# Kernel optimization log

Hardware: AMD Instinct MI355X
Metric: run time of the kernel (lower is better)

## Reference

```python
import jax, jax.numpy as jnp
import numpy as np

RADIUS = 0.2
K = 32  # num_neighbors


def ball_query(centers, points, radius, k):
    """centers [B,3,M], points [B,3,N] -> int32 indices [B,M,k].
    Matches PointNet++ CUDA semantics: first k points (in original order)
    with squared distance < radius^2; slots beyond the count are filled
    with the first valid index (0 if no point is in the ball)."""
    cn = jnp.sum(centers * centers, axis=1)              # [B,M]
    pn = jnp.sum(points * points, axis=1)                # [B,N]
    cross = jnp.einsum('bdm,bdn->bmn', centers, points)  # [B,M,N]
    d2 = cn[:, :, None] + pn[:, None, :] - 2.0 * cross   # [B,M,N]
    valid = d2 < radius * radius
    # stable argsort puts valid indices first, preserving original order
    order = jnp.argsort(jnp.logical_not(valid), axis=-1, stable=True)
    idx = order[..., :k]                                  # [B,M,k]
    count = jnp.sum(valid, axis=-1, keepdims=True)        # [B,M,1]
    fill = idx[..., :1]                                   # first valid (or 0)
    return jnp.where(jnp.arange(k)[None, None, :] < count, idx, fill)


def group(features, idx):
    """features [B,C,N], idx [B,M,K] -> [B,C,M,K]."""
    return jax.vmap(lambda f, i: jnp.take(f, i, axis=1))(features, idx)


def setup_inputs() -> dict:
    key = jax.random.key(0)
    k1, k2, k3, k4 = jax.random.split(key, 4)
    B, N, M, C, CT = 8, 8192, 2048, 64, 64
    return {
        'points_coords': jax.random.uniform(k1, (B, 3, N), dtype=jnp.float32),
        'centers_coords': jax.random.uniform(k2, (B, 3, M), dtype=jnp.float32),
        'temb': jax.random.normal(k3, (B, CT, N), dtype=jnp.float32),
        'points_features': jax.random.normal(k4, (B, C, N), dtype=jnp.float32),
    }


def reference(points_coords, centers_coords, temb, points_features):
    idx = ball_query(centers_coords, points_coords, RADIUS, K)           # [B,M,K]
    neighbor_coords = group(points_coords, idx) - centers_coords[:, :, :, None]  # [B,3,M,K]
    neighbor_features = jnp.concatenate(
        [neighbor_coords, group(points_features, idx)], axis=1)          # [B,3+C,M,K]
    temb_grouped = group(temb, idx)                                      # [B,CT,M,K]
    return neighbor_features, temb_grouped
```

## Files before the change

### kernel.cpp

```cpp
#include <hip/hip_runtime.h>

#define B  8
#define N  8192
#define M  2048
#define C  64
#define CT 64
#define K  32
#define R2 0.04f

__global__ __launch_bounds__(256) void transpose_kernel(
    const float* __restrict__ points,
    const float* __restrict__ temb,
    const float* __restrict__ feats,
    float* __restrict__ pointsT,
    float* __restrict__ tembT,
    float* __restrict__ featsT)
{
    const int gx = blockIdx.x;
    if (gx < 2048) {
        const int a  = gx >> 10;
        const int tt = gx & 1023;
        const int b  = tt >> 7;
        const int n0 = (tt & 127) << 6;
        const float* src = (a ? temb : feats) + (size_t)b * 64 * N;
        float* dst = (a ? tembT : featsT) + (size_t)b * N * 64;
        __shared__ float lds[64][65];
        const int nl = threadIdx.x & 63;
        const int c0 = threadIdx.x >> 6;
        #pragma unroll
        for (int i = 0; i < 16; ++i) {
            const int c = c0 + i * 4;
            lds[c][nl] = src[(size_t)c * N + n0 + nl];
        }
        __syncthreads();
        #pragma unroll
        for (int i = 0; i < 16; ++i) {
            const int n = c0 + i * 4;
            dst[(size_t)(n0 + n) * 64 + nl] = lds[nl][n];
        }
    } else {
        const int tt = gx - 2048;
        const int b  = tt >> 5;
        const int n  = ((tt & 31) << 8) + threadIdx.x;
        const float* pc = points + (size_t)b * 3 * N;
        float* dst = pointsT + ((size_t)b * N + n) * 4;
        const float px = pc[n];
        const float py = pc[N + n];
        const float pz = pc[2 * N + n];
        dst[0] = px;
        dst[1] = py;
        dst[2] = pz;
        dst[3] = __fadd_rn(__fadd_rn(__fmul_rn(px, px), __fmul_rn(py, py)),
                           __fmul_rn(pz, pz));
    }
}

#define PROC(vv, nn)                                                          \
    do {                                                                      \
        const float cross = __fadd_rn(                                        \
            __fadd_rn(__fmul_rn(cx, (vv).x), __fmul_rn(cy, (vv).y)),          \
            __fmul_rn(cz, (vv).z));                                           \
        const float d2 = __fsub_rn(__fadd_rn(cn, (vv).w),                     \
                                   __fmul_rn(2.0f, cross));                   \
        const bool valid = d2 < R2;                                           \
        const unsigned long long mask = __ballot(valid);                      \
        if (valid) {                                                          \
            const int slot = cnt + __builtin_amdgcn_mbcnt_hi(                 \
                (unsigned)(mask >> 32),                                       \
                __builtin_amdgcn_mbcnt_lo((unsigned)mask, 0));                \
            if (slot < K) snp[slot] = (nn);                                   \
        }                                                                     \
        cnt += (int)__popcll(mask);                                           \
    } while (0)

__global__ __launch_bounds__(256) void ball_query_kernel(
    const float* __restrict__ pointsT,
    const float* __restrict__ centers,
    int* __restrict__ idx)
{
    __shared__ int sidx[4][K];
    const int wave = threadIdx.x >> 6;
    const int lane = threadIdx.x & 63;
    const int center_id = blockIdx.x * 4 + wave;
    const int b = center_id >> 11;
    const int m = center_id & (M - 1);

    const float cx = centers[((size_t)b * 3 + 0) * M + m];
    const float cy = centers[((size_t)b * 3 + 1) * M + m];
    const float cz = centers[((size_t)b * 3 + 2) * M + m];
    const float cn = __fadd_rn(__fadd_rn(__fmul_rn(cx, cx), __fmul_rn(cy, cy)),
                               __fmul_rn(cz, cz));

    int* snp = sidx[wave];
    if (lane == 0) snp[0] = 0;

    const float4* pt4 = (const float4*)(pointsT + (size_t)b * N * 4);
    int cnt = 0;
    float4 va[4], vb[4];
    #pragma unroll
    for (int j = 0; j < 4; ++j) va[j] = pt4[j * 64 + lane];

    for (int g = 0; g < 32; g += 2) {
        if (g + 1 < 32) {
            #pragma unroll
            for (int j = 0; j < 4; ++j)
                vb[j] = pt4[((g + 1) * 4 + j) * 64 + lane];
        }
        #pragma unroll
        for (int j = 0; j < 4; ++j) PROC(va[j], g * 256 + j * 64 + lane);
        if (cnt >= K || g + 1 >= 32) break;

        if (g + 2 < 32) {
            #pragma unroll
            for (int j = 0; j < 4; ++j)
                va[j] = pt4[((g + 2) * 4 + j) * 64 + lane];
        }
        #pragma unroll
        for (int j = 0; j < 4; ++j) PROC(vb[j], (g + 1) * 256 + j * 64 + lane);
        if (cnt >= K) break;
    }

    if (lane < K) {
        const int fill = snp[0];
        const int v    = snp[lane];
        idx[(size_t)center_id * K + lane] = (lane < cnt) ? v : fill;
    }
}

__global__ __launch_bounds__(256) void gather_kernel(
    const float* __restrict__ pointsT,
    const float* __restrict__ centers,
    const float* __restrict__ tembT,
    const float* __restrict__ featsT,
    const int* __restrict__ idx,
    float* __restrict__ out1,
    float* __restrict__ out2)
{
    __shared__ int   sn[128];
    __shared__ float tile[128 * 65];
    __shared__ float ctile[3][128];

    const int t = threadIdx.x;
    const int MB4 = M / 4;
    const int b  = blockIdx.x / MB4;
    const int m0 = (blockIdx.x - b * MB4) * 4;
    const size_t base_mk = (size_t)m0 * K;
    const size_t cs = (size_t)M * K;

    if (t < 128) sn[t] = idx[((size_t)b * M + m0) * K + t];
    __syncthreads();

    const int cq = t & 15;
    const int pl = t >> 4;
    const float* fT = featsT + (size_t)b * N * 64;
    const float* tT = tembT  + (size_t)b * N * 64;

    #pragma unroll
    for (int i = 0; i < 8; ++i) {
        const int p = i * 16 + pl;
        const int n = sn[p];
        const float4 v = *(const float4*)(fT + (size_t)n * 64 + cq * 4);
        float* d = &tile[p * 65 + cq * 4];
        d[0] = v.x; d[1] = v.y; d[2] = v.z; d[3] = v.w;
    }
    __syncthreads();
    {
        const int p   = t & 127;
        const int ch0 = t >> 7;
        float* o = out1 + (size_t)b * 67 * cs + 3 * cs + base_mk + p;
        #pragma unroll
        for (int i = 0; i < 32; ++i) {
            const int c = ch0 + i * 2;
            o[(size_t)c * cs] = tile[p * 65 + c];
        }
    }
    __syncthreads();

    #pragma unroll
    for (int i = 0; i < 8; ++i) {
        const int p = i * 16 + pl;
        const int n = sn[p];
        const float4 v = *(const float4*)(tT + (size_t)n * 64 + cq * 4);
        float* d = &tile[p * 65 + cq * 4];
        d[0] = v.x; d[1] = v.y; d[2] = v.z; d[3] = v.w;
    }
    __syncthreads();
    {
        const int p   = t & 127;
        const int ch0 = t >> 7;
        float* o = out2 + (size_t)b * 64 * cs + base_mk + p;
        #pragma unroll
        for (int i = 0; i < 32; ++i) {
            const int c = ch0 + i * 2;
            o[(size_t)c * cs] = tile[p * 65 + c];
        }
    }

    if (t < 128) {
        const int p = t;
        const int n = sn[p];
        const int m = m0 + (p >> 5);
        const float4 v = *(const float4*)(pointsT + ((size_t)b * N + n) * 4);
        ctile[0][p] = v.x - centers[((size_t)b * 3 + 0) * M + m];
        ctile[1][p] = v.y - centers[((size_t)b * 3 + 1) * M + m];
        ctile[2][p] = v.z - centers[((size_t)b * 3 + 2) * M + m];
    }
    __syncthreads();
    {
        const int c = t >> 7;
        const int p = t & 127;
        out1[((size_t)b * 67 + c) * cs + base_mk + p] = ctile[c][p];
    }
    if (t < 128) {
        out1[((size_t)b * 67 + 2) * cs + base_mk + t] = ctile[2][t];
    }
}

extern "C" void kernel_launch(void* const* d_in, const int* in_sizes, int n_in,
                              void* d_out, int out_size, void* d_ws, size_t ws_size,
                              hipStream_t stream) {
    const float* points  = (const float*)d_in[0];
    const float* centers = (const float*)d_in[1];
    const float* temb    = (const float*)d_in[2];
    const float* feats   = (const float*)d_in[3];

    int*   idx     = (int*)d_ws;
    float* pointsT = (float*)((char*)d_ws + (2u << 20));
    float* featsT  = pointsT + (size_t)B * N * 4;
    float* tembT   = featsT  + (size_t)B * N * 64;

    float* out1 = (float*)d_out;
    float* out2 = out1 + (size_t)B * (3 + C) * M * K;

    transpose_kernel<<<2304, 256, 0, stream>>>(points, temb, feats,
                                               pointsT, tembT, featsT);
    ball_query_kernel<<<(B * M) / 4, 256, 0, stream>>>(pointsT, centers, idx);
    gather_kernel<<<(B * M) / 4, 256, 0, stream>>>(pointsT, centers, tembT,
                                                   featsT, idx, out1, out2);
}
```

Before: 334.9 us.

## Process four centers per wave in ball query to reuse loaded points

```diff
diff --git a/kernel.cpp b/kernel.cpp
--- a/kernel.cpp
+++ b/kernel.cpp
@@ -7,6 +7,13 @@
 #define CT 64
 #define K  32
 #define R2 0.04f
+
+__device__ __forceinline__ float rfl(float x) {
+    union { float f; int i; } u;
+    u.f = x;
+    u.i = __builtin_amdgcn_readfirstlane(u.i);
+    return u.f;
+}
 
 __global__ __launch_bounds__(256) void transpose_kernel(
     const float* __restrict__ points,
@@ -55,22 +62,35 @@
     }
 }
 
-#define PROC(vv, nn)                                                          \
+#define PROC1(vv, nn, c)                                                      \
     do {                                                                      \
         const float cross = __fadd_rn(                                        \
-            __fadd_rn(__fmul_rn(cx, (vv).x), __fmul_rn(cy, (vv).y)),          \
-            __fmul_rn(cz, (vv).z));                                           \
-        const float d2 = __fsub_rn(__fadd_rn(cn, (vv).w),                     \
+            __fadd_rn(__fmul_rn(cx[c], (vv).x), __fmul_rn(cy[c], (vv).y)),    \
+            __fmul_rn(cz[c], (vv).z));                                        \
+        const float d2 = __fsub_rn(__fadd_rn(cn[c], (vv).w),                  \
                                    __fmul_rn(2.0f, cross));                   \
         const bool valid = d2 < R2;                                           \
         const unsigned long long mask = __ballot(valid);                      \
         if (valid) {                                                          \
-            const int slot = cnt + __builtin_amdgcn_mbcnt_hi(                 \
+            const int slot = cnt[c] + __builtin_amdgcn_mbcnt_hi(              \
                 (unsigned)(mask >> 32),                                       \
                 __builtin_amdgcn_mbcnt_lo((unsigned)mask, 0));                \
-            if (slot < K) snp[slot] = (nn);                                   \
+            if (slot < K) sidx[wv4 + (c)][slot] = (nn);                       \
         }                                                                     \
-        cnt += (int)__popcll(mask);                                           \
+        cnt[c] += (int)__popcll(mask);                                        \
+    } while (0)
+
+#define GROUP(bf, gbase)                                                      \
+    do {                                                                      \
+        _Pragma("unroll")                                                     \
+        for (int c = 0; c < 4; ++c) {                                         \
+            if (cnt[c] < K) {                                                 \
+                PROC1(bf[0], (gbase) + 0 * 64 + lane, c);                     \
+                PROC1(bf[1], (gbase) + 1 * 64 + lane, c);                     \
+                PROC1(bf[2], (gbase) + 2 * 64 + lane, c);                     \
+                PROC1(bf[3], (gbase) + 3 * 64 + lane, c);                     \
+            }                                                                 \
+        }                                                                     \
     } while (0)
 
 __global__ __launch_bounds__(256) void ball_query_kernel(
@@ -78,24 +98,33 @@
     const float* __restrict__ centers,
     int* __restrict__ idx)
 {
-    __shared__ int sidx[4][K];
-    const int wave = threadIdx.x >> 6;
+    __shared__ int sidx[16][K];
+    const int wv   = threadIdx.x >> 6;
     const int lane = threadIdx.x & 63;
-    const int center_id = blockIdx.x * 4 + wave;
-    const int b = center_id >> 11;
-    const int m = center_id & (M - 1);
-
-    const float cx = centers[((size_t)b * 3 + 0) * M + m];
-    const float cy = centers[((size_t)b * 3 + 1) * M + m];
-    const float cz = centers[((size_t)b * 3 + 2) * M + m];
-    const float cn = __fadd_rn(__fadd_rn(__fmul_rn(cx, cx), __fmul_rn(cy, cy)),
-                               __fmul_rn(cz, cz));
-
-    int* snp = sidx[wave];
-    if (lane == 0) snp[0] = 0;
+    const int wv4  = wv * 4;
+    const int cid0 = blockIdx.x * 16 + wv4;
+    const int b    = cid0 >> 11;
+    const int m0c  = cid0 & (M - 1);
+
+    float cx[4], cy[4], cz[4], cn[4];
+    #pragma unroll
+    for (int c = 0; c < 4; ++c) {
+        const int m = m0c + c;
+        cx[c] = rfl(centers[((size_t)b * 3 + 0) * M + m]);
+        cy[c] = rfl(centers[((size_t)b * 3 + 1) * M + m]);
+        cz[c] = rfl(centers[((size_t)b * 3 + 2) * M + m]);
+        cn[c] = rfl(__fadd_rn(
+            __fadd_rn(__fmul_rn(cx[c], cx[c]), __fmul_rn(cy[c], cy[c])),
+            __fmul_rn(cz[c], cz[c])));
+    }
+
+    if (lane == 0) {
+        #pragma unroll
+        for (int c = 0; c < 4; ++c) sidx[wv4 + c][0] = 0;
+    }
 
     const float4* pt4 = (const float4*)(pointsT + (size_t)b * N * 4);
-    int cnt = 0;
+    int cnt[4] = {0, 0, 0, 0};
     float4 va[4], vb[4];
     #pragma unroll
     for (int j = 0; j < 4; ++j) va[j] = pt4[j * 64 + lane];
@@ -106,24 +135,26 @@
             for (int j = 0; j < 4; ++j)
                 vb[j] = pt4[((g + 1) * 4 + j) * 64 + lane];
         }
-        #pragma unroll
-        for (int j = 0; j < 4; ++j) PROC(va[j], g * 256 + j * 64 + lane);
-        if (cnt >= K || g + 1 >= 32) break;
+        GROUP(va, g * 256);
+        if ((cnt[0] >= K && cnt[1] >= K && cnt[2] >= K && cnt[3] >= K) ||
+            g + 1 >= 32) break;
 
         if (g + 2 < 32) {
             #pragma unroll
             for (int j = 0; j < 4; ++j)
                 va[j] = pt4[((g + 2) * 4 + j) * 64 + lane];
         }
-        #pragma unroll
-        for (int j = 0; j < 4; ++j) PROC(vb[j], (g + 1) * 256 + j * 64 + lane);
-        if (cnt >= K) break;
-    }
-
-    if (lane < K) {
-        const int fill = snp[0];
-        const int v    = snp[lane];
-        idx[(size_t)center_id * K + lane] = (lane < cnt) ? v : fill;
+        GROUP(vb, (g + 1) * 256);
+        if (cnt[0] >= K && cnt[1] >= K && cnt[2] >= K && cnt[3] >= K) break;
+    }
+
+    #pragma unroll
+    for (int c = 0; c < 4; ++c) {
+        if (lane < K) {
+            const int fill = sidx[wv4 + c][0];
+            const int v    = sidx[wv4 + c][lane];
+            idx[(size_t)(cid0 + c) * K + lane] = (lane < cnt[c]) ? v : fill;
+        }
     }
 }
 
@@ -234,7 +265,7 @@
 
     transpose_kernel<<<2304, 256, 0, stream>>>(points, temb, feats,
                                                pointsT, tembT, featsT);
-    ball_query_kernel<<<(B * M) / 4, 256, 0, stream>>>(pointsT, centers, idx);
+    ball_query_kernel<<<(B * M) / 16, 256, 0, stream>>>(pointsT, centers, idx);
     gather_kernel<<<(B * M) / 4, 256, 0, stream>>>(pointsT, centers, tembT,
                                                    featsT, idx, out1, out2);
 }
```

Result: no change. 334.1 us (-0.2%).

## Fuse ball query into gather kernel and halve shared tile size

Applied to the files above, without the earlier changes.

```diff
diff --git a/kernel.cpp b/kernel.cpp
--- a/kernel.cpp
+++ b/kernel.cpp
@@ -7,6 +7,13 @@
 #define CT 64
 #define K  32
 #define R2 0.04f
+
+__device__ __forceinline__ float rfl(float x) {
+    union { float f; int i; } u;
+    u.f = x;
+    u.i = __builtin_amdgcn_readfirstlane(u.i);
+    return u.f;
+}
 
 __global__ __launch_bounds__(256) void transpose_kernel(
     const float* __restrict__ points,
@@ -73,71 +80,16 @@
         cnt += (int)__popcll(mask);                                           \
     } while (0)
 
-__global__ __launch_bounds__(256) void ball_query_kernel(
-    const float* __restrict__ pointsT,
-    const float* __restrict__ centers,
-    int* __restrict__ idx)
-{
-    __shared__ int sidx[4][K];
-    const int wave = threadIdx.x >> 6;
-    const int lane = threadIdx.x & 63;
-    const int center_id = blockIdx.x * 4 + wave;
-    const int b = center_id >> 11;
-    const int m = center_id & (M - 1);
-
-    const float cx = centers[((size_t)b * 3 + 0) * M + m];
-    const float cy = centers[((size_t)b * 3 + 1) * M + m];
-    const float cz = centers[((size_t)b * 3 + 2) * M + m];
-    const float cn = __fadd_rn(__fadd_rn(__fmul_rn(cx, cx), __fmul_rn(cy, cy)),
-                               __fmul_rn(cz, cz));
-
-    int* snp = sidx[wave];
-    if (lane == 0) snp[0] = 0;
-
-    const float4* pt4 = (const float4*)(pointsT + (size_t)b * N * 4);
-    int cnt = 0;
-    float4 va[4], vb[4];
-    #pragma unroll
-    for (int j = 0; j < 4; ++j) va[j] = pt4[j * 64 + lane];
-
-    for (int g = 0; g < 32; g += 2) {
-        if (g + 1 < 32) {
-            #pragma unroll
-            for (int j = 0; j < 4; ++j)
-                vb[j] = pt4[((g + 1) * 4 + j) * 64 + lane];
-        }
-        #pragma unroll
-        for (int j = 0; j < 4; ++j) PROC(va[j], g * 256 + j * 64 + lane);
-        if (cnt >= K || g + 1 >= 32) break;
-
-        if (g + 2 < 32) {
-            #pragma unroll
-            for (int j = 0; j < 4; ++j)
-                va[j] = pt4[((g + 2) * 4 + j) * 64 + lane];
-        }
-        #pragma unroll
-        for (int j = 0; j < 4; ++j) PROC(vb[j], (g + 1) * 256 + j * 64 + lane);
-        if (cnt >= K) break;
-    }
-
-    if (lane < K) {
-        const int fill = snp[0];
-        const int v    = snp[lane];
-        idx[(size_t)center_id * K + lane] = (lane < cnt) ? v : fill;
-    }
-}
-
-__global__ __launch_bounds__(256) void gather_kernel(
+__global__ __launch_bounds__(256, 8) void fused_kernel(
     const float* __restrict__ pointsT,
     const float* __restrict__ centers,
     const float* __restrict__ tembT,
     const float* __restrict__ featsT,
-    const int* __restrict__ idx,
     float* __restrict__ out1,
     float* __restrict__ out2)
 {
     __shared__ int   sn[128];
-    __shared__ float tile[128 * 65];
+    __shared__ float tile[64 * 65];
     __shared__ float ctile[3][128];
 
     const int t = threadIdx.x;
@@ -147,7 +99,52 @@
     const size_t base_mk = (size_t)m0 * K;
     const size_t cs = (size_t)M * K;
 
-    if (t < 128) sn[t] = idx[((size_t)b * M + m0) * K + t];
+    {
+        const int wv   = t >> 6;
+        const int lane = t & 63;
+        const int m    = m0 + wv;
+        const float cx = rfl(centers[((size_t)b * 3 + 0) * M + m]);
+        const float cy = rfl(centers[((size_t)b * 3 + 1) * M + m]);
+        const float cz = rfl(centers[((size_t)b * 3 + 2) * M + m]);
+        const float cn = rfl(__fadd_rn(
+            __fadd_rn(__fmul_rn(cx, cx), __fmul_rn(cy, cy)),
+            __fmul_rn(cz, cz)));
+
+        int* snp = &sn[wv * K];
+        if (lane == 0) snp[0] = 0;
+
+        const float4* pt4 = (const float4*)(pointsT + (size_t)b * N * 4);
+        int cnt = 0;
+        float4 va[4], vb[4];
+        #pragma unroll
+        for (int j = 0; j < 4; ++j) va[j] = pt4[j * 64 + lane];
+
+        for (int g = 0; g < 32; g += 2) {
+            if (g + 1 < 32) {
+                #pragma unroll
+                for (int j = 0; j < 4; ++j)
+                    vb[j] = pt4[((g + 1) * 4 + j) * 64 + lane];
+            }
+            #pragma unroll
+            for (int j = 0; j < 4; ++j) PROC(va[j], g * 256 + j * 64 + lane);
+            if (cnt >= K || g + 1 >= 32) break;
+
+            if (g + 2 < 32) {
+                #pragma unroll
+                for (int j = 0; j < 4; ++j)
+                    va[j] = pt4[((g + 2) * 4 + j) * 64 + lane];
+            }
+            #pragma unroll
+            for (int j = 0; j < 4; ++j) PROC(vb[j], (g + 1) * 256 + j * 64 + lane);
+            if (cnt >= K) break;
+        }
+
+        if (lane < K) {
+            const int fill = snp[0];
+            const int v    = snp[lane];
+            snp[lane] = (lane < cnt) ? v : fill;
+        }
+    }
     __syncthreads();
 
     const int cq = t & 15;
@@ -156,44 +153,51 @@
     const float* tT = tembT  + (size_t)b * N * 64;
 
     #pragma unroll
-    for (int i = 0; i < 8; ++i) {
-        const int p = i * 16 + pl;
-        const int n = sn[p];
-        const float4 v = *(const float4*)(fT + (size_t)n * 64 + cq * 4);
-        float* d = &tile[p * 65 + cq * 4];
-        d[0] = v.x; d[1] = v.y; d[2] = v.z; d[3] = v.w;
-    }
-    __syncthreads();
-    {
-        const int p   = t & 127;
-        const int ch0 = t >> 7;
-        float* o = out1 + (size_t)b * 67 * cs + 3 * cs + base_mk + p;
-        #pragma unroll
-        for (int i = 0; i < 32; ++i) {
-            const int c = ch0 + i * 2;
-            o[(size_t)c * cs] = tile[p * 65 + c];
-        }
-    }
-    __syncthreads();
+    for (int h = 0; h < 2; ++h) {
+        #pragma unroll
+        for (int i = 0; i < 4; ++i) {
+            const int pr = i * 16 + pl;
+            const int n  = sn[h * 64 + pr];
+            const float4 v = *(const float4*)(fT + (size_t)n * 64 + cq * 4);
+            float* d = &tile[pr * 65 + cq * 4];
+            d[0] = v.x; d[1] = v.y; d[2] = v.z; d[3] = v.w;
+        }
+        __syncthreads();
+        {
+            const int p   = t & 63;
+            const int ch0 = t >> 6;
+            float* o = out1 + (size_t)b * 67 * cs + 3 * cs + base_mk + h * 64 + p;
+            #pragma unroll
+            for (int i = 0; i < 16; ++i) {
+                const int c = ch0 + i * 4;
+                o[(size_t)c * cs] = tile[p * 65 + c];
+            }
+        }
+        __syncthreads();
+    }
 
     #pragma unroll
-    for (int i = 0; i < 8; ++i) {
-        const int p = i * 16 + pl;
-        const int n = sn[p];
-        const float4 v = *(const float4*)(tT + (size_t)n * 64 + cq * 4);
-        float* d = &tile[p * 65 + cq * 4];
-        d[0] = v.x; d[1] = v.y; d[2] = v.z; d[3] = v.w;
-    }
-    __syncthreads();
-    {
-        const int p   = t & 127;
-        const int ch0 = t >> 7;
-        float* o = out2 + (size_t)b * 64 * cs + base_mk + p;
-        #pragma unroll
-        for (int i = 0; i < 32; ++i) {
-            const int c = ch0 + i * 2;
-            o[(size_t)c * cs] = tile[p * 65 + c];
-        }
+    for (int h = 0; h < 2; ++h) {
+        #pragma unroll
+        for (int i = 0; i < 4; ++i) {
+            const int pr = i * 16 + pl;
+            const int n  = sn[h * 64 + pr];
+            const float4 v = *(const float4*)(tT + (size_t)n * 64 + cq * 4);
+            float* d = &tile[pr * 65 + cq * 4];
+            d[0] = v.x; d[1] = v.y; d[2] = v.z; d[3] = v.w;
+        }
+        __syncthreads();
+        {
+            const int p   = t & 63;
+            const int ch0 = t >> 6;
+            float* o = out2 + (size_t)b * 64 * cs + base_mk + h * 64 + p;
+            #pragma unroll
+            for (int i = 0; i < 16; ++i) {
+                const int c = ch0 + i * 4;
+                o[(size_t)c * cs] = tile[p * 65 + c];
+            }
+        }
+        __syncthreads();
     }
 
     if (t < 128) {
@@ -224,8 +228,7 @@
     const float* temb    = (const float*)d_in[2];
     const float* feats   = (const float*)d_in[3];
 
-    int*   idx     = (int*)d_ws;
-    float* pointsT = (float*)((char*)d_ws + (2u << 20));
+    float* pointsT = (float*)d_ws;
     float* featsT  = pointsT + (size_t)B * N * 4;
     float* tembT   = featsT  + (size_t)B * N * 64;
 
@@ -234,7 +237,6 @@
 
     transpose_kernel<<<2304, 256, 0, stream>>>(points, temb, feats,
                                                pointsT, tembT, featsT);
-    ball_query_kernel<<<(B * M) / 4, 256, 0, stream>>>(pointsT, centers, idx);
-    gather_kernel<<<(B * M) / 4, 256, 0, stream>>>(pointsT, centers, tembT,
-                                                   featsT, idx, out1, out2);
-}
+    fused_kernel<<<(B * M) / 4, 256, 0, stream>>>(pointsT, centers, tembT,
+                                                  featsT, out1, out2);
+}
```

After: 353.5 us. 5.6% more time.

## Fuse ball query into gather kernel, keeping neighbor indices in shared memory

Applied to the files above, without the earlier changes.

```diff
diff --git a/kernel.cpp b/kernel.cpp
--- a/kernel.cpp
+++ b/kernel.cpp
@@ -7,6 +7,13 @@
 #define CT 64
 #define K  32
 #define R2 0.04f
+
+__device__ __forceinline__ float rfl(float x) {
+    union { float f; int i; } u;
+    u.f = x;
+    u.i = __builtin_amdgcn_readfirstlane(u.i);
+    return u.f;
+}
 
 __global__ __launch_bounds__(256) void transpose_kernel(
     const float* __restrict__ points,
@@ -73,66 +80,11 @@
         cnt += (int)__popcll(mask);                                           \
     } while (0)
 
-__global__ __launch_bounds__(256) void ball_query_kernel(
-    const float* __restrict__ pointsT,
-    const float* __restrict__ centers,
-    int* __restrict__ idx)
-{
-    __shared__ int sidx[4][K];
-    const int wave = threadIdx.x >> 6;
-    const int lane = threadIdx.x & 63;
-    const int center_id = blockIdx.x * 4 + wave;
-    const int b = center_id >> 11;
-    const int m = center_id & (M - 1);
-
-    const float cx = centers[((size_t)b * 3 + 0) * M + m];
-    const float cy = centers[((size_t)b * 3 + 1) * M + m];
-    const float cz = centers[((size_t)b * 3 + 2) * M + m];
-    const float cn = __fadd_rn(__fadd_rn(__fmul_rn(cx, cx), __fmul_rn(cy, cy)),
-                               __fmul_rn(cz, cz));
-
-    int* snp = sidx[wave];
-    if (lane == 0) snp[0] = 0;
-
-    const float4* pt4 = (const float4*)(pointsT + (size_t)b * N * 4);
-    int cnt = 0;
-    float4 va[4], vb[4];
-    #pragma unroll
-    for (int j = 0; j < 4; ++j) va[j] = pt4[j * 64 + lane];
-
-    for (int g = 0; g < 32; g += 2) {
-        if (g + 1 < 32) {
-            #pragma unroll
-            for (int j = 0; j < 4; ++j)
-                vb[j] = pt4[((g + 1) * 4 + j) * 64 + lane];
-        }
-        #pragma unroll
-        for (int j = 0; j < 4; ++j) PROC(va[j], g * 256 + j * 64 + lane);
-        if (cnt >= K || g + 1 >= 32) break;
-
-        if (g + 2 < 32) {
-            #pragma unroll
-            for (int j = 0; j < 4; ++j)
-                va[j] = pt4[((g + 2) * 4 + j) * 64 + lane];
-        }
-        #pragma unroll
-        for (int j = 0; j < 4; ++j) PROC(vb[j], (g + 1) * 256 + j * 64 + lane);
-        if (cnt >= K) break;
-    }
-
-    if (lane < K) {
-        const int fill = snp[0];
-        const int v    = snp[lane];
-        idx[(size_t)center_id * K + lane] = (lane < cnt) ? v : fill;
-    }
-}
-
-__global__ __launch_bounds__(256) void gather_kernel(
+__global__ __launch_bounds__(256) void fused_kernel(
     const float* __restrict__ pointsT,
     const float* __restrict__ centers,
     const float* __restrict__ tembT,
     const float* __restrict__ featsT,
-    const int* __restrict__ idx,
     float* __restrict__ out1,
     float* __restrict__ out2)
 {
@@ -147,7 +99,52 @@
     const size_t base_mk = (size_t)m0 * K;
     const size_t cs = (size_t)M * K;
 
-    if (t < 128) sn[t] = idx[((size_t)b * M + m0) * K + t];
+    {
+        const int wv   = t >> 6;
+        const int lane = t & 63;
+        const int m    = m0 + wv;
+        const float cx = rfl(centers[((size_t)b * 3 + 0) * M + m]);
+        const float cy = rfl(centers[((size_t)b * 3 + 1) * M + m]);
+        const float cz = rfl(centers[((size_t)b * 3 + 2) * M + m]);
+        const float cn = rfl(__fadd_rn(
+            __fadd_rn(__fmul_rn(cx, cx), __fmul_rn(cy, cy)),
+            __fmul_rn(cz, cz)));
+
+        int* snp = &sn[wv * K];
+        if (lane == 0) snp[0] = 0;
+
+        const float4* pt4 = (const float4*)(pointsT + (size_t)b * N * 4);
+        int cnt = 0;
+        float4 va[4], vb[4];
+        #pragma unroll
+        for (int j = 0; j < 4; ++j) va[j] = pt4[j * 64 + lane];
+
+        for (int g = 0; g < 32; g += 2) {
+            if (g + 1 < 32) {
+                #pragma unroll
+                for (int j = 0; j < 4; ++j)
+                    vb[j] = pt4[((g + 1) * 4 + j) * 64 + lane];
+            }
+            #pragma unroll
+            for (int j = 0; j < 4; ++j) PROC(va[j], g * 256 + j * 64 + lane);
+            if (cnt >= K || g + 1 >= 32) break;
+
+            if (g + 2 < 32) {
+                #pragma unroll
+                for (int j = 0; j < 4; ++j)
+                    va[j] = pt4[((g + 2) * 4 + j) * 64 + lane];
+            }
+            #pragma unroll
+            for (int j = 0; j < 4; ++j) PROC(vb[j], (g + 1) * 256 + j * 64 + lane);
+            if (cnt >= K) break;
+        }
+
+        if (lane < K) {
+            const int fill = snp[0];
+            const int v    = snp[lane];
+            snp[lane] = (lane < cnt) ? v : fill;
+        }
+    }
     __syncthreads();
 
     const int cq = t & 15;
@@ -224,8 +221,7 @@
     const float* temb    = (const float*)d_in[2];
     const float* feats   = (const float*)d_in[3];
 
-    int*   idx     = (int*)d_ws;
-    float* pointsT = (float*)((char*)d_ws + (2u << 20));
+    float* pointsT = (float*)d_ws;
     float* featsT  = pointsT + (size_t)B * N * 4;
     float* tembT   = featsT  + (size_t)B * N * 64;
 
@@ -234,7 +230,6 @@
 
     transpose_kernel<<<2304, 256, 0, stream>>>(points, temb, feats,
                                                pointsT, tembT, featsT);
-    ball_query_kernel<<<(B * M) / 4, 256, 0, stream>>>(pointsT, centers, idx);
-    gather_kernel<<<(B * M) / 4, 256, 0, stream>>>(pointsT, centers, tembT,
-                                                   featsT, idx, out1, out2);
-}
+    fused_kernel<<<(B * M) / 4, 256, 0, stream>>>(pointsT, centers, tembT,
+                                                  featsT, out1, out2);
+}
```

Measured after the change: 328.3 us. -2.0%, faster.
